# Optimization experiments

Hardware: AMD Instinct MI355X
Metric: run time of the kernel (lower is better)

## Reference

```python
import jax, jax.numpy as jnp
import numpy as np

N, E, G, H, L = 50000, 400000, 2000, 128, 5
NPG = N // G  # 25 nodes per graph
EPS = 1e-5    # PNA std epsilon
D_LOG = 1.0   # avg_d['log'] as in 3DInfomax PNAGNN


def setup_inputs():
    key = jax.random.key(0)
    ks = jax.random.split(key, 32)
    node_feat = jax.random.randint(ks[0], (N, 9), 0, 16)
    edge_feat = jax.random.randint(ks[1], (E, 3), 0, 5)
    src = jax.random.randint(ks[2], (E,), 0, N)
    off = jax.random.randint(ks[3], (E,), 1, NPG)
    # dst stays in the same graph as src and differs from src
    dst = (src // NPG) * NPG + (src % NPG + off) % NPG
    graph_id = jnp.arange(N) // NPG
    inp = dict(node_feat=node_feat, edge_feat=edge_feat, src=src, dst=dst,
               graph_id=graph_id)
    shapes = [("aemb_f", (144, H)), ("bemb_f", (15, H)),
              ("w_pre_f", (L, 3 * H, H)), ("b_pre_f", (L, H)),
              ("w_post_f", (L, 13 * H, H)), ("b_post_f", (L, H)),
              ("w_out3", (3 * H, 256)), ("b_out3", (256,)),
              ("aemb", (144, H)), ("bemb", (15, H)),
              ("w_pre", (L, 3 * H, H)), ("b_pre", (L, H)),
              ("w_post", (L, 13 * H, H)), ("b_post", (L, H)),
              ("w1", (3 * H + 256, H)), ("b1", (H,)),
              ("w2", (H, 128)), ("b2", (128,))]
    for i, (n, s) in enumerate(shapes):
        inp[n] = jax.random.normal(ks[4 + i], s, dtype=jnp.float32) * 0.05
    return inp


def _embed(table, x, vocab):
    # sum of per-feature embeddings (OGB Atom/Bond encoder)
    idx = x + jnp.arange(x.shape[1]) * vocab
    return table[idx].sum(axis=1)


def _pna_gnn(aemb, bemb, w_pre, b_pre, w_post, b_post,
             node_feat, edge_feat, src, dst):
    h = _embed(aemb, node_feat, 16)   # [N, H]
    e = _embed(bemb, edge_feat, 5)    # [E, H]
    deg = jax.ops.segment_sum(jnp.ones((src.shape[0],), jnp.float32), dst, N)
    safe_deg = jnp.maximum(deg, 1.0)[:, None]
    log_deg = jnp.log(deg + 1.0)[:, None]
    amp = log_deg / D_LOG                                   # amplification scaler
    att = jnp.where(log_deg > 0, D_LOG / jnp.where(log_deg > 0, log_deg, 1.0), 0.0)
    has_in = (deg > 0)[:, None]
    for l in range(L):
        h_in = h
        # pretrans over edges: cat(src, dst, edge) -> linear (pretrans_layers=1, last_activation='none')
        z = jnp.concatenate([h[src], h[dst], e], axis=-1) @ w_pre[l] + b_pre[l]  # [E, H]
        s1 = jax.ops.segment_sum(z, dst, N)
        mean = s1 / safe_deg
        mean_sq = jax.ops.segment_sum(z * z, dst, N) / safe_deg
        std = jnp.sqrt(jax.nn.relu(mean_sq - mean * mean) + EPS)
        mx = jnp.where(has_in, jax.ops.segment_max(z, dst, N), 0.0)
        mn = jnp.where(has_in, jax.ops.segment_min(z, dst, N), 0.0)
        agg = jnp.concatenate([mean, mx, mn, std], axis=-1)          # [N, 4H]
        f = jnp.concatenate([agg, agg * amp, agg * att], axis=-1)    # [N, 12H]
        f = jnp.where(has_in, f, 0.0)  # DGL leaves zero-in-degree nodes at zero
        h = jnp.concatenate([h, f], axis=-1) @ w_post[l] + b_post[l]
        h = h + h_in  # residual
    return h


def _readout(h, graph_id):
    mean = jax.ops.segment_sum(h, graph_id, G) / NPG
    mx = jax.ops.segment_max(h, graph_id, G)
    mn = jax.ops.segment_min(h, graph_id, G)
    return jnp.concatenate([mn, mx, mean], axis=-1)  # order: min, max, mean


def reference(aemb_f, bemb_f, w_pre_f, b_pre_f, w_post_f, b_post_f,
              w_out3, b_out3, aemb, bemb, w_pre, b_pre, w_post, b_post,
              w1, b1, w2, b2, node_feat, edge_feat, src, dst, graph_id):
    # frozen 3D branch (torch.no_grad + detach -> stop_gradient)
    h3 = _pna_gnn(aemb_f, bemb_f, w_pre_f, b_pre_f, w_post_f, b_post_f,
                  node_feat, edge_feat, src, dst)
    r3 = _readout(h3, graph_id)
    latent3d = jax.lax.stop_gradient(r3 @ w_out3 + b_out3)  # [G, 256]
    # trainable 2D branch
    h2 = _pna_gnn(aemb, bemb, w_pre, b_pre, w_post, b_post,
                  node_feat, edge_feat, src, dst)
    r2 = _readout(h2, graph_id)                              # [G, 384]
    x = jnp.concatenate([r2, latent3d], axis=-1)             # [G, 640]
    h1 = jax.nn.relu(x @ w1 + b1)
    return h1 @ w2 + b2                                      # [G, 128]
```

## Files before the change

kernel.cpp:

```cpp
#include <hip/hip_runtime.h>
#include <hip/hip_bf16.h>
#include <math.h>

#define Nn 50000
#define Ee 400000
#define Gg 2000
#define NPGc 25
#define Hc 128
#define Lc 5
#define M2c 50048
#define R2c 100096

typedef __attribute__((ext_vector_type(8))) short short8;
typedef __attribute__((ext_vector_type(4))) float fx4;

__device__ inline short bf16r(float x){
  unsigned u = __float_as_uint(x);
  unsigned r = (u + 0x7fffu + ((u >> 16) & 1u)) >> 16;
  return (short)r;
}
__device__ inline float bf16f(short s){
  return __uint_as_float(((unsigned)(unsigned short)s) << 16);
}

__global__ void deg_kernel(const int* __restrict__ dst, int* __restrict__ deg, int E){
  int i = blockIdx.x * blockDim.x + threadIdx.x;
  if (i < E) atomicAdd(&deg[dst[i]], 1);
}

__global__ void scan1_kernel(const int* __restrict__ deg, int* __restrict__ part,
                             int* __restrict__ bsums, int n){
  __shared__ int tmp[1024];
  int b = blockIdx.x, t = threadIdx.x;
  int i = b * 1024 + t;
  int v = (i < n) ? deg[i] : 0;
  tmp[t] = v;
  __syncthreads();
  for (int off = 1; off < 1024; off <<= 1){
    int add = (t >= off) ? tmp[t - off] : 0;
    __syncthreads();
    tmp[t] += add;
    __syncthreads();
  }
  part[i] = tmp[t];
  if (t == 1023) bsums[b] = tmp[1023];
}
__global__ void scan2_kernel(int* __restrict__ bsums, int nb){
  if (threadIdx.x == 0){
    int s = 0;
    for (int i = 0; i < nb; i++){ s += bsums[i]; bsums[i] = s; }
  }
}
__global__ void scan3_kernel(const int* __restrict__ part, const int* __restrict__ bsums,
                             int* __restrict__ rowstart, int n){
  int i = blockIdx.x * blockDim.x + threadIdx.x;
  if (i == 0) rowstart[0] = 0;
  if (i < n){
    int b = i >> 10;
    int base = b ? bsums[b - 1] : 0;
    rowstart[i + 1] = part[i] + base;
  }
}

__global__ void copy_int_kernel(const int* __restrict__ a, int* __restrict__ b, int n){
  int i = blockIdx.x * blockDim.x + threadIdx.x;
  if (i < n) b[i] = a[i];
}

__global__ void scatter_kernel(const int* __restrict__ src, const int* __restrict__ dst,
                               const int* __restrict__ ef, int* cursor,
                               int* __restrict__ pk_srt, int E){
  int i = blockIdx.x * blockDim.x + threadIdx.x;
  if (i >= E) return;
  int p = atomicAdd(&cursor[dst[i]], 1);
  int code = ef[i * 3 + 0] * 25 + ef[i * 3 + 1] * 5 + ef[i * 3 + 2];
  pk_srt[p] = (code << 16) | (src[i] % NPGc);
}

__global__ void ampatt_kernel(const int* __restrict__ deg, float* __restrict__ amp,
                              float* __restrict__ att, int n){
  int i = blockIdx.x * blockDim.x + threadIdx.x;
  if (i >= n) return;
  if (i >= Nn){ amp[i] = 0.f; att[i] = 0.f; return; }
  float d = (float)deg[i];
  float ld = logf(d + 1.0f);
  amp[i] = ld;
  att[i] = (deg[i] > 0) ? (1.0f / ld) : 0.0f;
}

__global__ void embed2_kernel(const int* __restrict__ nf,
                              const float* __restrict__ aemb_f,
                              const float* __restrict__ aemb_t,
                              float* __restrict__ h, short* __restrict__ h16){
  int idx = blockIdx.x * blockDim.x + threadIdx.x;
  if (idx >= R2c * Hc) return;
  int n = idx >> 7, c = idx & 127;
  int br = n >= M2c;
  int local = n - br * M2c;
  if (local >= Nn){ h[idx] = 0.f; h16[idx] = 0; return; }
  const float* aemb = br ? aemb_t : aemb_f;
  float s = 0.f;
#pragma unroll
  for (int f = 0; f < 9; f++){
    int row = nf[local * 9 + f] + 16 * f;
    s += aemb[row * Hc + c];
  }
  h[idx] = s;
  h16[idx] = bf16r(s);
}

__global__ void bsum2_kernel(const float* __restrict__ bemb_f, const float* __restrict__ bemb_t,
                             float* __restrict__ bsum2){
  int idx = blockIdx.x * blockDim.x + threadIdx.x;
  if (idx >= 2 * 125 * Hc) return;
  int b = idx / (125 * Hc);
  int rem = idx % (125 * Hc);
  int code = rem >> 7, c = rem & 127;
  int e0 = code / 25, e1 = (code / 5) % 5, e2 = code % 5;
  const float* bemb = b ? bemb_t : bemb_f;
  bsum2[idx] = bemb[e0 * Hc + c] + bemb[(5 + e1) * Hc + c] + bemb[(10 + e2) * Hc + c];
}

__global__ void conv_pre_all_kernel(const float* __restrict__ wpre_f,
                                    const float* __restrict__ wpre_t,
                                    short* __restrict__ btpre_all){
  int idx = blockIdx.x * blockDim.x + threadIdx.x;
  if (idx >= 2 * Lc * 256 * 128) return;
  int bl = idx / (256 * 128);
  int rem = idx % (256 * 128);
  int col = rem >> 7, k = rem & 127;
  int b = bl / Lc, l = bl % Lc;
  const float* wl = (b ? wpre_t : wpre_f) + (size_t)l * 384 * 128;
  float v = (col < 128) ? wl[k * 128 + col] : wl[(128 + k) * 128 + (col - 128)];
  btpre_all[(size_t)bl * 256 * 128 + col * 128 + k] = bf16r(v);
}
__global__ void conv_post_all_kernel(const float* __restrict__ wpost_f,
                                     const float* __restrict__ wpost_t,
                                     short* __restrict__ btpost_all){
  int idx = blockIdx.x * blockDim.x + threadIdx.x;
  if (idx >= 2 * Lc * 1664 * 128) return;
  int bl = idx / (1664 * 128);
  int rem = idx % (1664 * 128);
  int k = rem >> 7, c = rem & 127;
  int b = bl / Lc, l = bl % Lc;
  const float* wl = (b ? wpost_t : wpost_f) + (size_t)l * 1664 * 128;
  btpost_all[(size_t)bl * 128 * 1664 + (size_t)c * 1664 + k] = bf16r(wl[(size_t)k * 128 + c]);
}

__global__ void ezt_all_kernel(const float* __restrict__ wpre_f, const float* __restrict__ wpre_t,
                               const float* __restrict__ bpre_f, const float* __restrict__ bpre_t,
                               const float* __restrict__ bsum2, short* __restrict__ ezt16_all){
  int code = blockIdx.x;
  int bl   = blockIdx.y;
  int t = threadIdx.x;
  int b = bl / Lc, l = bl % Lc;
  const float* wl = (b ? wpre_t : wpre_f) + (size_t)l * 384 * 128 + 256 * 128;
  const float* bp = (b ? bpre_t : bpre_f) + (size_t)l * 128;
  __shared__ float bs[128];
  bs[t] = bsum2[((size_t)b * 125 + code) * 128 + t];
  __syncthreads();
  float acc = bp[t];
#pragma unroll 8
  for (int k = 0; k < 128; k++) acc += bs[k] * wl[k * 128 + t];
  ezt16_all[((size_t)bl * 125 + code) * 128 + t] = bf16r(acc);
}

__global__ void readout2_kernel(const float* __restrict__ h,
                                float* __restrict__ r3, float* __restrict__ r2){
  int bi = blockIdx.x;
  int br = bi >= Gg;
  int g = bi - br * Gg;
  int c = threadIdx.x;
  float mn = 3.402823466e38f, mx = -3.402823466e38f, s = 0.f;
  const float* hp = h + ((size_t)br * M2c + (size_t)g * NPGc) * Hc + c;
#pragma unroll
  for (int i = 0; i < NPGc; i++){
    float v = hp[i * Hc];
    mn = fminf(mn, v); mx = fmaxf(mx, v); s += v;
  }
  float* r = br ? r2 : r3;
  r[(size_t)g * 384 + c]       = mn;
  r[(size_t)g * 384 + 128 + c] = mx;
  r[(size_t)g * 384 + 256 + c] = s * (1.0f / NPGc);
}

__global__ __launch_bounds__(256)
void head_kernel(const float* __restrict__ r2, const float* __restrict__ r3,
                 const float* __restrict__ w_out3, const float* __restrict__ b_out3,
                 const float* __restrict__ w1, const float* __restrict__ b1,
                 const float* __restrict__ w2, const float* __restrict__ b2,
                 float* __restrict__ out)
{
  __shared__ float r3_s[384];
  __shared__ float x_s[640];
  __shared__ float h1_s[128];
  __shared__ float partial[256];
  int g = blockIdx.x, t = threadIdx.x;

  for (int i = t; i < 384; i += 256){
    float v2 = r2[(size_t)g * 384 + i];
    r3_s[i] = r3[(size_t)g * 384 + i];
    x_s[i] = v2;
  }
  __syncthreads();

  {
    float acc = b_out3[t];
#pragma unroll 8
    for (int k = 0; k < 384; k++) acc += r3_s[k] * w_out3[k * 256 + t];
    x_s[384 + t] = acc;
  }
  __syncthreads();

  {
    int c = t & 127, half = t >> 7;
    float acc = half ? 0.f : b1[c];
    int kb = half * 320;
#pragma unroll 8
    for (int k = kb; k < kb + 320; k++) acc += x_s[k] * w1[k * 128 + c];
    partial[t] = acc;
  }
  __syncthreads();
  if (t < 128) h1_s[t] = fmaxf(partial[t] + partial[t + 128], 0.f);
  __syncthreads();

  {
    int c = t & 127, half = t >> 7;
    float acc = half ? 0.f : b2[c];
    int kb = half * 64;
#pragma unroll 8
    for (int k = kb; k < kb + 64; k++) acc += h1_s[k] * w2[k * 128 + c];
    partial[t] = acc;
  }
  __syncthreads();
  if (t < 128) out[(size_t)g * 128 + t] = partial[t] + partial[t + 128];
}

__global__ __launch_bounds__(256, 4)
void fgemm_agg_kernel(const short* __restrict__ h16,
                      const short* __restrict__ pre0, const short* __restrict__ pre1,
                      const int* __restrict__ ez0, const int* __restrict__ ez1,
                      const int* __restrict__ pk_srt, const int* __restrict__ rowstart,
                      short* __restrict__ aggG)
{
  __shared__ short h_s[32 * 128];
  __shared__ short hsd_s[32 * 256];

  int tid = threadIdx.x;
  int bi = blockIdx.x;
  int brn = bi >= Gg;
  int g = bi - brn * Gg;
  const short* h16b = h16 + (size_t)brn * M2c * 128;
  const short* Bt = brn ? pre1 : pre0;
  const int* ez16 = brn ? ez1 : ez0;
  short* aggOut = aggG + (size_t)brn * M2c * 512;
  int base = g * NPGc;

  {
    const int* src = (const int*)(h16b + (size_t)base * 128);
    int* dst = (int*)h_s;
    for (int t = tid; t < NPGc * 64; t += 256){
      int row = t >> 6, ci = t & 63;
      dst[row * 64 + (ci ^ ((row & 7) << 2))] = src[t];
    }
  }
  __syncthreads();

  int wv = tid >> 6, ln = tid & 63;
  int l15 = ln & 15, lq = ln >> 4;
  {
    fx4 acc[2][4];
#pragma unroll
    for (int mt = 0; mt < 2; mt++)
#pragma unroll
      for (int ct = 0; ct < 4; ct++) acc[mt][ct] = (fx4){0.f, 0.f, 0.f, 0.f};

    short8 af[2][4];
#pragma unroll
    for (int mt = 0; mt < 2; mt++){
      int row = mt * 16 + l15;
#pragma unroll
      for (int ks = 0; ks < 4; ks++){
        int sk = ks * 32 + lq * 8;
        af[mt][ks] = *(const short8*)(h_s + row * 128 + (sk ^ ((row & 7) << 3)));
      }
    }
#pragma unroll
    for (int ks = 0; ks < 4; ks++){
#pragma unroll
      for (int ct = 0; ct < 4; ct++){
        int col = wv * 64 + ct * 16 + l15;
        short8 bf = *(const short8*)(Bt + (size_t)col * 128 + ks * 32 + lq * 8);
        acc[0][ct] = __builtin_amdgcn_mfma_f32_16x16x32_bf16(af[0][ks], bf, acc[0][ct], 0, 0, 0);
        acc[1][ct] = __builtin_amdgcn_mfma_f32_16x16x32_bf16(af[1][ks], bf, acc[1][ct], 0, 0, 0);
      }
    }
#pragma unroll
    for (int mt = 0; mt < 2; mt++){
#pragma unroll
      for (int ct = 0; ct < 4; ct++){
        int cc = wv * 64 + ct * 16 + l15;
#pragma unroll
        for (int r = 0; r < 4; r++){
          int row = mt * 16 + lq * 4 + r;
          hsd_s[row * 256 + (cc ^ ((row & 7) << 3))] = bf16r(acc[mt][ct][r]);
        }
      }
    }
  }
  __syncthreads();

  int sub = tid & 15;
  int go = sub * 4;
  const int* hsd_i = (const int*)hsd_s;

#pragma unroll
  for (int rnd = 0; rnd < 2; rnd++){
    int nd = rnd * 16 + (tid >> 4);
    if (nd >= NPGc) continue;
    int node = base + nd;
    int e0 = rowstart[node], e1 = rowstart[node + 1];
    short* o = aggOut + (size_t)node * 512 + sub * 8;
    if (e1 <= e0){
      short8 z = {0, 0, 0, 0, 0, 0, 0, 0};
      *(short8*)(o)       = z;
      *(short8*)(o + 128) = z;
      *(short8*)(o + 256) = z;
      *(short8*)(o + 384) = z;
      continue;
    }

    float hdv[8];
    {
      int4 hd = *(const int4*)(hsd_i + nd * 128 + ((64 + go) ^ ((nd & 7) << 2)));
      const int* hp = (const int*)&hd;
#pragma unroll
      for (int i = 0; i < 4; i++){
        hdv[2 * i]     = __uint_as_float(((unsigned)hp[i]) << 16);
        hdv[2 * i + 1] = __uint_as_float(((unsigned)hp[i]) & 0xffff0000u);
      }
    }

    float sum[8], sq[8], mx[8], mn[8];
#pragma unroll
    for (int j = 0; j < 8; j++){
      sum[j] = 0.f; sq[j] = 0.f;
      mx[j] = -3.402823466e38f; mn[j] = 3.402823466e38f;
    }

    for (int k = e0; k < e1; k += 4){
      int pk[4];
#pragma unroll
      for (int t2 = 0; t2 < 4; t2++){
        int kk = (k + t2 < e1) ? (k + t2) : (e1 - 1);
        pk[t2] = pk_srt[kk];
      }
      int4 ev[4], hv[4];
#pragma unroll
      for (int t2 = 0; t2 < 4; t2++){
        int s = pk[t2] & 0xffff;
        ev[t2] = *(const int4*)(ez16 + (pk[t2] >> 16) * 64 + go);
        hv[t2] = *(const int4*)(hsd_i + s * 128 + (go ^ ((s & 7) << 2)));
      }
#pragma unroll
      for (int t2 = 0; t2 < 4; t2++){
        if (k + t2 < e1){
          const int* pp = (const int*)&hv[t2];
          const int* ee = (const int*)&ev[t2];
#pragma unroll
          for (int i = 0; i < 4; i++){
            float z0 = __uint_as_float(((unsigned)pp[i]) << 16) + hdv[2 * i]
                     + __uint_as_float(((unsigned)ee[i]) << 16);
            float z1 = __uint_as_float(((unsigned)pp[i]) & 0xffff0000u) + hdv[2 * i + 1]
                     + __uint_as_float(((unsigned)ee[i]) & 0xffff0000u);
            sum[2 * i] += z0;     sq[2 * i] += z0 * z0;
            mx[2 * i] = fmaxf(mx[2 * i], z0); mn[2 * i] = fminf(mn[2 * i], z0);
            sum[2 * i + 1] += z1; sq[2 * i + 1] += z1 * z1;
            mx[2 * i + 1] = fmaxf(mx[2 * i + 1], z1); mn[2 * i + 1] = fminf(mn[2 * i + 1], z1);
          }
        }
      }
    }

    float d = (float)(e1 - e0);
    float rd = 1.0f / d;
    short8 sm, sx, sn, sd;
#pragma unroll
    for (int j = 0; j < 8; j++){
      float m = sum[j] * rd;
      float v = sq[j] * rd - m * m; v = v > 0.f ? v : 0.f;
      sm[j] = bf16r(m);
      sx[j] = bf16r(mx[j]);
      sn[j] = bf16r(mn[j]);
      sd[j] = bf16r(sqrtf(v + 1e-5f));
    }
    *(short8*)(o)       = sm;
    *(short8*)(o + 128) = sx;
    *(short8*)(o + 256) = sn;
    *(short8*)(o + 384) = sd;
  }
}

__global__ __launch_bounds__(256, 4)
void post_gemm_kernel(const short* __restrict__ A16,
                      const short* __restrict__ aggG,
                      const short* __restrict__ Bt0, const short* __restrict__ Bt1,
                      const float* __restrict__ bias0, const float* __restrict__ bias1,
                      const float* __restrict__ amp, const float* __restrict__ att,
                      const float* __restrict__ resid,
                      float* __restrict__ C, short* __restrict__ C16)
{
  __shared__ short8 As[1024];
  __shared__ short8 Bs[512];

  int tid = threadIdx.x;
  int row0 = blockIdx.y * 128;
  int col0 = blockIdx.x * 64;
  int br = row0 >= M2c;
  const short* Bt = br ? Bt1 : Bt0;
  const float* bias = br ? bias1 : bias0;
  int wv = tid >> 6, ln = tid & 63;
  int lo = ln & 15, q = ln >> 4;

  int a_rq = (tid >> 6) & 3, a_q = (tid >> 4) & 3, a_lo = tid & 15;
  int b_q = (tid >> 4) & 3, b_lo = tid & 15, b_ct = (tid >> 6) & 3;

  int arow[2]; float ampv[2], attv[2];
#pragma unroll
  for (int j = 0; j < 2; j++){
    arow[j] = row0 + (a_rq + 4 * j) * 16 + a_lo;
    int lr = arow[j] - br * M2c;
    ampv[j] = amp[lr]; attv[j] = att[lr];
  }
  size_t colb = (size_t)(col0 + b_ct * 16 + b_lo) * 1664;

  fx4 acc[2][4];
#pragma unroll
  for (int j = 0; j < 2; j++)
#pragma unroll
    for (int ct = 0; ct < 4; ct++) acc[j][ct] = (fx4){0.f, 0.f, 0.f, 0.f};

  short8 ra[2][2], rb[2];
  auto loadA = [&](int s){
    if (s < 2){
#pragma unroll
      for (int i = 0; i < 2; i++){
        int k = s * 64 + i * 32 + a_q * 8;
#pragma unroll
        for (int j = 0; j < 2; j++)
          ra[i][j] = *(const short8*)(A16 + (size_t)arow[j] * 128 + k);
      }
    } else {
      int kc = (s - 2) / 3;
#pragma unroll
      for (int i = 0; i < 2; i++){
        int koff = kc * 64 + i * 32 + a_q * 8;
#pragma unroll
        for (int j = 0; j < 2; j++)
          ra[i][j] = *(const short8*)(aggG + (size_t)arow[j] * 512 + koff);
      }
    }
  };
  auto loadB = [&](int s){
    int gkb;
    if (s < 2) gkb = s * 64;
    else {
      int t = s - 2, kc = t / 3, ph = t % 3;
      gkb = (ph == 0 ? 128 : (ph == 1 ? 640 : 1152)) + kc * 64;
    }
#pragma unroll
    for (int i = 0; i < 2; i++)
      rb[i] = *(const short8*)(Bt + colb + gkb + i * 32 + b_q * 8);
  };

  loadA(0); loadB(0);
  for (int s = 0; s < 26; s++){
    int ph = (s < 2) ? 0 : (s - 2) % 3;
    __syncthreads();
    if (ph == 0){
#pragma unroll
      for (int i = 0; i < 2; i++)
#pragma unroll
        for (int j = 0; j < 2; j++) As[i * 512 + j * 256 + tid] = ra[i][j];
    } else {
#pragma unroll
      for (int i = 0; i < 2; i++)
#pragma unroll
        for (int j = 0; j < 2; j++){
          float sc = (ph == 1) ? ampv[j] : attv[j];
          short8 v = ra[i][j];
#pragma unroll
          for (int e = 0; e < 8; e++)
            ((short*)&v)[e] = bf16r(bf16f(((short*)&v)[e]) * sc);
          As[i * 512 + j * 256 + tid] = v;
        }
    }
#pragma unroll
    for (int i = 0; i < 2; i++) Bs[i * 256 + tid] = rb[i];
    __syncthreads();
    if (s < 25){
      loadB(s + 1);
      if (s + 1 < 2 || (s - 1) % 3 == 0) loadA(s + 1);
    }
    short8 a00 = As[wv * 64 + ln];
    short8 a10 = As[512 + wv * 64 + ln];
    short8 a01 = As[256 + wv * 64 + ln];
    short8 a11 = As[768 + wv * 64 + ln];
#pragma unroll
    for (int ct = 0; ct < 4; ct++){
      short8 b0 = Bs[ct * 64 + ln];
      short8 b1 = Bs[256 + ct * 64 + ln];
      acc[0][ct] = __builtin_amdgcn_mfma_f32_16x16x32_bf16(a00, b0, acc[0][ct], 0, 0, 0);
      acc[0][ct] = __builtin_amdgcn_mfma_f32_16x16x32_bf16(a10, b1, acc[0][ct], 0, 0, 0);
      acc[1][ct] = __builtin_amdgcn_mfma_f32_16x16x32_bf16(a01, b0, acc[1][ct], 0, 0, 0);
      acc[1][ct] = __builtin_amdgcn_mfma_f32_16x16x32_bf16(a11, b1, acc[1][ct], 0, 0, 0);
    }
  }

#pragma unroll
  for (int j = 0; j < 2; j++){
#pragma unroll
    for (int ct = 0; ct < 4; ct++){
      int col = col0 + ct * 16 + lo;
      float bcol = bias[col];
#pragma unroll
      for (int r = 0; r < 4; r++){
        int row = row0 + (wv + 4 * j) * 16 + q * 4 + r;
        float v = acc[j][ct][r] + bcol + resid[(size_t)row * 128 + col];
        C[(size_t)row * 128 + col] = v;
        C16[(size_t)row * 128 + col] = bf16r(v);
      }
    }
  }
}

extern "C" void kernel_launch(void* const* d_in, const int* in_sizes, int n_in,
                              void* d_out, int out_size, void* d_ws, size_t ws_size,
                              hipStream_t stream)
{
  const int*   node_feat = (const int*)  d_in[0];
  const int*   edge_feat = (const int*)  d_in[1];
  const int*   src       = (const int*)  d_in[2];
  const int*   dst       = (const int*)  d_in[3];
  const float* aemb_f  = (const float*) d_in[5];
  const float* bemb_f  = (const float*) d_in[6];
  const float* w_pre_f = (const float*) d_in[7];
  const float* b_pre_f = (const float*) d_in[8];
  const float* w_post_f= (const float*) d_in[9];
  const float* b_post_f= (const float*) d_in[10];
  const float* w_out3  = (const float*) d_in[11];
  const float* b_out3  = (const float*) d_in[12];
  const float* aemb    = (const float*) d_in[13];
  const float* bemb    = (const float*) d_in[14];
  const float* w_pre   = (const float*) d_in[15];
  const float* b_pre   = (const float*) d_in[16];
  const float* w_post  = (const float*) d_in[17];
  const float* b_post  = (const float*) d_in[18];
  const float* w1      = (const float*) d_in[19];
  const float* b1      = (const float*) d_in[20];
  const float* w2      = (const float*) d_in[21];
  const float* b2      = (const float*) d_in[22];
  float* out = (float*)d_out;

  char* w = (char*)d_ws;
  auto carve = [&](size_t bytes) -> void* {
    void* p = (void*)w;
    w += (bytes + 255) & ~(size_t)255;
    return p;
  };
  float* h         = (float*)carve((size_t)R2c * Hc * 4);
  short* h16_a     = (short*)carve((size_t)R2c * Hc * 2);
  short* h16_b     = (short*)carve((size_t)R2c * Hc * 2);
  short* aggG      = (short*)carve((size_t)R2c * 512 * 2);
  short* btpre_all = (short*)carve((size_t)2 * Lc * 256 * 128 * 2);
  short* btpost_all= (short*)carve((size_t)2 * Lc * 128 * 1664 * 2);
  short* ezt16_all = (short*)carve((size_t)2 * Lc * 125 * Hc * 2);
  float* amp       = (float*)carve((size_t)M2c * 4);
  float* att       = (float*)carve((size_t)M2c * 4);
  int* rowstart = (int*)carve((size_t)(Nn + 1) * 4);
  int* pk_srt   = (int*)carve((size_t)Ee * 4);

  char* ali = (char*)aggG;
  float* r3     = (float*)(ali);
  float* r2     = (float*)(ali + (size_t)4 * 1024 * 1024);
  int*   deg    = (int*)  (ali + (size_t)8 * 1024 * 1024);
  int*   cursor = (int*)  (ali + (size_t)9 * 1024 * 1024);
  int*   part   = (int*)  (ali + (size_t)10 * 1024 * 1024);
  int*   bsums  = (int*)  (ali + (size_t)11 * 1024 * 1024);
  float* bsum2  = (float*)(ali + (size_t)12 * 1024 * 1024);

  hipMemsetAsync(deg, 0, (size_t)Nn * 4, stream);
  deg_kernel<<<(Ee + 255) / 256, 256, 0, stream>>>(dst, deg, Ee);
  scan1_kernel<<<49, 1024, 0, stream>>>(deg, part, bsums, Nn);
  scan2_kernel<<<1, 64, 0, stream>>>(bsums, 49);
  scan3_kernel<<<(Nn + 255) / 256, 256, 0, stream>>>(part, bsums, rowstart, Nn);
  copy_int_kernel<<<(Nn + 255) / 256, 256, 0, stream>>>(rowstart, cursor, Nn);
  scatter_kernel<<<(Ee + 255) / 256, 256, 0, stream>>>(src, dst, edge_feat, cursor,
                                                       pk_srt, Ee);
  ampatt_kernel<<<(M2c + 255) / 256, 256, 0, stream>>>(deg, amp, att, M2c);

  hipMemsetAsync(aggG + (size_t)Nn * 512, 0, (size_t)(M2c - Nn) * 512 * 2, stream);
  hipMemsetAsync(aggG + ((size_t)M2c + Nn) * 512, 0, (size_t)(M2c - Nn) * 512 * 2, stream);

  bsum2_kernel<<<(2 * 125 * Hc + 255) / 256, 256, 0, stream>>>(bemb_f, bemb, bsum2);
  conv_pre_all_kernel<<<(2 * Lc * 256 * 128 + 255) / 256, 256, 0, stream>>>(
      w_pre_f, w_pre, btpre_all);
  conv_post_all_kernel<<<(2 * Lc * 1664 * 128 + 255) / 256, 256, 0, stream>>>(
      w_post_f, w_post, btpost_all);
  ezt_all_kernel<<<dim3(125, 2 * Lc), 128, 0, stream>>>(
      w_pre_f, w_pre, b_pre_f, b_pre, bsum2, ezt16_all);

  short* g_cur = h16_a;
  short* g_nxt = h16_b;
  embed2_kernel<<<(R2c * Hc + 255) / 256, 256, 0, stream>>>(
      node_feat, aemb_f, aemb, h, g_cur);

  for (int l = 0; l < Lc; l++){
    const short* pre0 = btpre_all + (size_t)(0 * Lc + l) * 256 * 128;
    const short* pre1 = btpre_all + (size_t)(1 * Lc + l) * 256 * 128;
    const short* post0 = btpost_all + (size_t)(0 * Lc + l) * 128 * 1664;
    const short* post1 = btpost_all + (size_t)(1 * Lc + l) * 128 * 1664;
    const int* ez0 = (const int*)(ezt16_all + (size_t)(0 * Lc + l) * 125 * Hc);
    const int* ez1 = (const int*)(ezt16_all + (size_t)(1 * Lc + l) * 125 * Hc);
    const float* bp0 = b_post_f + (size_t)l * 128;
    const float* bp1 = b_post   + (size_t)l * 128;

    fgemm_agg_kernel<<<2 * Gg, 256, 0, stream>>>(
        g_cur, pre0, pre1, ez0, ez1, pk_srt, rowstart, aggG);

    post_gemm_kernel<<<dim3(2, R2c / 128), 256, 0, stream>>>(
        g_cur, aggG, post0, post1, bp0, bp1, amp, att, h, h, g_nxt);

    { short* t = g_cur; g_cur = g_nxt; g_nxt = t; }
  }

  readout2_kernel<<<2 * Gg, 128, 0, stream>>>(h, r3, r2);
  head_kernel<<<Gg, 256, 0, stream>>>(r2, r3, w_out3, b_out3, w1, b1, w2, b2, out);
}
```

Baseline: 1.202 ms.

## Factor amp/att scalers out of post GEMM into three accumulators

The post-transform GEMM no longer rescales the aggregated A tile by the per-row amplification and attenuation factors before each MMA. It keeps three accumulator sets: one for the unscaled product, one for the amp-weighted product and one for the att-weighted product. The same A tile is reused against three B slices per step, and the per-row scalers are applied once in the epilogue. This removes per-element bf16 rescaling and cuts the K loop from 26 to 10 steps with fewer A loads, but triples the accumulator registers and B shared memory, and occupancy drops from 4 to 3 blocks per CU. Rounding also changes slightly because the scaling moves from the bf16 inputs to the fp32 accumulators.

```diff
diff --git a/kernel.cpp b/kernel.cpp
--- a/kernel.cpp
+++ b/kernel.cpp
@@ -401,7 +401,7 @@
   }
 }
 
-__global__ __launch_bounds__(256, 4)
+__global__ __launch_bounds__(256, 3)
 void post_gemm_kernel(const short* __restrict__ A16,
                       const short* __restrict__ aggG,
                       const short* __restrict__ Bt0, const short* __restrict__ Bt1,
@@ -411,7 +411,7 @@
                       float* __restrict__ C, short* __restrict__ C16)
 {
   __shared__ short8 As[1024];
-  __shared__ short8 Bs[512];
+  __shared__ short8 Bs[1536];
 
   int tid = threadIdx.x;
   int row0 = blockIdx.y * 128;
@@ -425,22 +425,20 @@
   int a_rq = (tid >> 6) & 3, a_q = (tid >> 4) & 3, a_lo = tid & 15;
   int b_q = (tid >> 4) & 3, b_lo = tid & 15, b_ct = (tid >> 6) & 3;
 
-  int arow[2]; float ampv[2], attv[2];
-#pragma unroll
-  for (int j = 0; j < 2; j++){
-    arow[j] = row0 + (a_rq + 4 * j) * 16 + a_lo;
-    int lr = arow[j] - br * M2c;
-    ampv[j] = amp[lr]; attv[j] = att[lr];
-  }
+  int arow[2];
+#pragma unroll
+  for (int j = 0; j < 2; j++) arow[j] = row0 + (a_rq + 4 * j) * 16 + a_lo;
   size_t colb = (size_t)(col0 + b_ct * 16 + b_lo) * 1664;
 
-  fx4 acc[2][4];
-#pragma unroll
-  for (int j = 0; j < 2; j++)
-#pragma unroll
-    for (int ct = 0; ct < 4; ct++) acc[j][ct] = (fx4){0.f, 0.f, 0.f, 0.f};
-
-  short8 ra[2][2], rb[2];
+  fx4 acc[3][2][4];
+#pragma unroll
+  for (int sec = 0; sec < 3; sec++)
+#pragma unroll
+    for (int j = 0; j < 2; j++)
+#pragma unroll
+      for (int ct = 0; ct < 4; ct++) acc[sec][j][ct] = (fx4){0.f, 0.f, 0.f, 0.f};
+
+  short8 ra[2][2], rb[3][2];
   auto loadA = [&](int s){
     if (s < 2){
 #pragma unroll
@@ -451,7 +449,7 @@
           ra[i][j] = *(const short8*)(A16 + (size_t)arow[j] * 128 + k);
       }
     } else {
-      int kc = (s - 2) / 3;
+      int kc = s - 2;
 #pragma unroll
       for (int i = 0; i < 2; i++){
         int koff = kc * 64 + i * 32 + a_q * 8;
@@ -462,46 +460,41 @@
     }
   };
   auto loadB = [&](int s){
-    int gkb;
-    if (s < 2) gkb = s * 64;
-    else {
-      int t = s - 2, kc = t / 3, ph = t % 3;
-      gkb = (ph == 0 ? 128 : (ph == 1 ? 640 : 1152)) + kc * 64;
-    }
+    if (s < 2){
+      int gkb = s * 64;
+#pragma unroll
+      for (int i = 0; i < 2; i++)
+        rb[0][i] = *(const short8*)(Bt + colb + gkb + i * 32 + b_q * 8);
+    } else {
+      int kc = s - 2;
+#pragma unroll
+      for (int sec = 0; sec < 3; sec++){
+        int gkb = (sec == 0 ? 128 : (sec == 1 ? 640 : 1152)) + kc * 64;
+#pragma unroll
+        for (int i = 0; i < 2; i++)
+          rb[sec][i] = *(const short8*)(Bt + colb + gkb + i * 32 + b_q * 8);
+      }
+    }
+  };
+
+  loadA(0); loadB(0);
+  for (int s = 0; s < 10; s++){
+    __syncthreads();
 #pragma unroll
     for (int i = 0; i < 2; i++)
-      rb[i] = *(const short8*)(Bt + colb + gkb + i * 32 + b_q * 8);
-  };
-
-  loadA(0); loadB(0);
-  for (int s = 0; s < 26; s++){
-    int ph = (s < 2) ? 0 : (s - 2) % 3;
+#pragma unroll
+      for (int j = 0; j < 2; j++) As[i * 512 + j * 256 + tid] = ra[i][j];
+    if (s < 2){
+#pragma unroll
+      for (int i = 0; i < 2; i++) Bs[i * 256 + tid] = rb[0][i];
+    } else {
+#pragma unroll
+      for (int sec = 0; sec < 3; sec++)
+#pragma unroll
+        for (int i = 0; i < 2; i++) Bs[sec * 512 + i * 256 + tid] = rb[sec][i];
+    }
     __syncthreads();
-    if (ph == 0){
-#pragma unroll
-      for (int i = 0; i < 2; i++)
-#pragma unroll
-        for (int j = 0; j < 2; j++) As[i * 512 + j * 256 + tid] = ra[i][j];
-    } else {
-#pragma unroll
-      for (int i = 0; i < 2; i++)
-#pragma unroll
-        for (int j = 0; j < 2; j++){
-          float sc = (ph == 1) ? ampv[j] : attv[j];
-          short8 v = ra[i][j];
-#pragma unroll
-          for (int e = 0; e < 8; e++)
-            ((short*)&v)[e] = bf16r(bf16f(((short*)&v)[e]) * sc);
-          As[i * 512 + j * 256 + tid] = v;
-        }
-    }
-#pragma unroll
-    for (int i = 0; i < 2; i++) Bs[i * 256 + tid] = rb[i];
-    __syncthreads();
-    if (s < 25){
-      loadB(s + 1);
-      if (s + 1 < 2 || (s - 1) % 3 == 0) loadA(s + 1);
-    }
+    if (s < 9){ loadA(s + 1); loadB(s + 1); }
     short8 a00 = As[wv * 64 + ln];
     short8 a10 = As[512 + wv * 64 + ln];
     short8 a01 = As[256 + wv * 64 + ln];
@@ -510,23 +503,47 @@
     for (int ct = 0; ct < 4; ct++){
       short8 b0 = Bs[ct * 64 + ln];
       short8 b1 = Bs[256 + ct * 64 + ln];
-      acc[0][ct] = __builtin_amdgcn_mfma_f32_16x16x32_bf16(a00, b0, acc[0][ct], 0, 0, 0);
-      acc[0][ct] = __builtin_amdgcn_mfma_f32_16x16x32_bf16(a10, b1, acc[0][ct], 0, 0, 0);
-      acc[1][ct] = __builtin_amdgcn_mfma_f32_16x16x32_bf16(a01, b0, acc[1][ct], 0, 0, 0);
-      acc[1][ct] = __builtin_amdgcn_mfma_f32_16x16x32_bf16(a11, b1, acc[1][ct], 0, 0, 0);
-    }
-  }
-
+      acc[0][0][ct] = __builtin_amdgcn_mfma_f32_16x16x32_bf16(a00, b0, acc[0][0][ct], 0, 0, 0);
+      acc[0][0][ct] = __builtin_amdgcn_mfma_f32_16x16x32_bf16(a10, b1, acc[0][0][ct], 0, 0, 0);
+      acc[0][1][ct] = __builtin_amdgcn_mfma_f32_16x16x32_bf16(a01, b0, acc[0][1][ct], 0, 0, 0);
+      acc[0][1][ct] = __builtin_amdgcn_mfma_f32_16x16x32_bf16(a11, b1, acc[0][1][ct], 0, 0, 0);
+    }
+    if (s >= 2){
+#pragma unroll
+      for (int sec = 1; sec < 3; sec++){
+#pragma unroll
+        for (int ct = 0; ct < 4; ct++){
+          short8 b0 = Bs[sec * 512 + ct * 64 + ln];
+          short8 b1 = Bs[sec * 512 + 256 + ct * 64 + ln];
+          acc[sec][0][ct] = __builtin_amdgcn_mfma_f32_16x16x32_bf16(a00, b0, acc[sec][0][ct], 0, 0, 0);
+          acc[sec][0][ct] = __builtin_amdgcn_mfma_f32_16x16x32_bf16(a10, b1, acc[sec][0][ct], 0, 0, 0);
+          acc[sec][1][ct] = __builtin_amdgcn_mfma_f32_16x16x32_bf16(a01, b0, acc[sec][1][ct], 0, 0, 0);
+          acc[sec][1][ct] = __builtin_amdgcn_mfma_f32_16x16x32_bf16(a11, b1, acc[sec][1][ct], 0, 0, 0);
+        }
+      }
+    }
+  }
+
+  int lrow0 = row0 - br * M2c;
 #pragma unroll
   for (int j = 0; j < 2; j++){
+    int rbase = (wv + 4 * j) * 16 + q * 4;
+    float ampr[4], attr[4];
+#pragma unroll
+    for (int r = 0; r < 4; r++){
+      ampr[r] = amp[lrow0 + rbase + r];
+      attr[r] = att[lrow0 + rbase + r];
+    }
 #pragma unroll
     for (int ct = 0; ct < 4; ct++){
       int col = col0 + ct * 16 + lo;
       float bcol = bias[col];
 #pragma unroll
       for (int r = 0; r < 4; r++){
-        int row = row0 + (wv + 4 * j) * 16 + q * 4 + r;
-        float v = acc[j][ct][r] + bcol + resid[(size_t)row * 128 + col];
+        int row = row0 + rbase + r;
+        float v = acc[0][j][ct][r] + ampr[r] * acc[1][j][ct][r]
+                + attr[r] * acc[2][j][ct][r] + bcol
+                + resid[(size_t)row * 128 + col];
         C[(size_t)row * 128 + col] = v;
         C16[(size_t)row * 128 + col] = bf16r(v);
       }
```

Result: slower. 1.514 ms (+25.9%).
